# Performance work log

Hardware: AMD Instinct MI355X
Metric: run time of the kernel (lower is better)

## Reference

```python
import jax, jax.numpy as jnp
import numpy as np

EPS = 1e-5
DIM = 128
SCALE = DIM ** (-0.5)


def setup_inputs() -> dict:
    key = jax.random.key(0)
    k1, k2, k3 = jax.random.split(key, 3)
    B, N, D = 2, 128 * 128, DIM
    Q = N // 4
    x = jax.random.normal(k1, (B, N, D), dtype=jnp.float32)
    gamma = jnp.ones((D,), dtype=jnp.float32)
    beta = jnp.zeros((D,), dtype=jnp.float32)
    queries = jax.random.normal(k2, (Q, D), dtype=jnp.float32)
    W = jax.random.normal(k3, (2 * D, D), dtype=jnp.float32) * (1.0 / np.sqrt(D))
    return {"x": x, "gamma": gamma, "beta": beta, "queries": queries, "W": W}


def reference(x, gamma, beta, queries, W):
    # LayerNorm over last dim (eps matches torch default 1e-5)
    mu = jnp.mean(x, axis=-1, keepdims=True)
    var = jnp.mean(jnp.square(x - mu), axis=-1, keepdims=True)
    xn = (x - mu) * jax.lax.rsqrt(var + EPS) * gamma + beta  # [B, N, D]
    # learned-query cross attention: sim = Q @ xn^T * scale -> softmax -> @ xn
    sim = jnp.einsum('qd,bnd->bqn', queries, xn) * SCALE     # [B, Q, N]
    attn = jax.nn.softmax(sim, axis=-1)
    out = jnp.einsum('bqn,bnd->bqd', attn, xn)               # [B, Q, D]
    # trailing linear: dim -> 2*dim, no bias
    return jnp.einsum('bqd,ed->bqe', out, W)                 # [B, Q, 2D]
```

## Files before the change

kernel.cpp:

```cpp
#include <hip/hip_runtime.h>
#include <stdint.h>

#define Bb 2
#define Nn 16384
#define Dd 128
#define Qq 4096
#define Ee 256
#define NSPLIT 8
#define NCHUNK 2048
#define KV 64
#define NITER 32

typedef __bf16 bf16x8 __attribute__((ext_vector_type(8)));
typedef float floatx4 __attribute__((ext_vector_type(4)));

__device__ __forceinline__ unsigned f2bf1(float f) {
  unsigned u = __float_as_uint(f);
  u = u + 0x7FFFu + ((u >> 16) & 1u);
  return u >> 16;
}
__device__ __forceinline__ unsigned f2bf2(float lo, float hi) {
  return f2bf1(lo) | (f2bf1(hi) << 16);
}

__global__ __launch_bounds__(256) void k_ln(const float* __restrict__ x,
    const float* __restrict__ gamma, const float* __restrict__ beta,
    unsigned* __restrict__ xn) {
  int row = blockIdx.x * 4 + (threadIdx.x >> 6);
  int lane = threadIdx.x & 63;
  float2 v = ((const float2*)x)[(size_t)row * 64 + lane];
  float s = v.x + v.y, s2 = v.x * v.x + v.y * v.y;
#pragma unroll
  for (int off = 32; off; off >>= 1) {
    s += __shfl_xor(s, off);
    s2 += __shfl_xor(s2, off);
  }
  float mu = s * (1.0f / 128.0f);
  float var = s2 * (1.0f / 128.0f) - mu * mu;
  float rs = rsqrtf(var + 1e-5f);
  float2 g = ((const float2*)gamma)[lane];
  float2 bt = ((const float2*)beta)[lane];
  float y0 = (v.x - mu) * rs * g.x + bt.x;
  float y1 = (v.y - mu) * rs * g.y + bt.y;
  xn[(size_t)row * 64 + lane] = f2bf2(y0, y1);
}

__global__ __launch_bounds__(256) void k_cast(const float* __restrict__ queries,
    const float* __restrict__ W, unsigned short* __restrict__ qb,
    unsigned short* __restrict__ wb) {
  int i = blockIdx.x * 256 + threadIdx.x;
  const float QSC = 0.08838834764831845f * 1.4426950408889634f;
  if (i < Qq * Dd) {
    qb[i] = (unsigned short)f2bf1(queries[i] * QSC);
  } else {
    int j = i - Qq * Dd;
    if (j < Ee * Dd) wb[j] = (unsigned short)f2bf1(W[j]);
  }
}

#define TSTRIDE 132
__global__ __launch_bounds__(256) void k_transpose(
    const unsigned short* __restrict__ xn, unsigned short* __restrict__ xnT) {
  __shared__ unsigned short lds[64 * TSTRIDE];
  int bid = blockIdx.x;
  int b = bid >> 8, nt = bid & 255;
  int n0 = nt * 64;
  int t = threadIdx.x;
#pragma unroll
  for (int p = 0; p < 4; ++p) {
    int u = p * 256 + t;
    int r = u >> 4, c = u & 15;
    uint4 d4 = *(const uint4*)(xn + ((size_t)(b * Nn + n0 + r) * Dd + c * 8));
    uint2* dst = (uint2*)&lds[r * TSTRIDE + c * 8];
    dst[0] = make_uint2(d4.x, d4.y);
    dst[1] = make_uint2(d4.z, d4.w);
  }
  __syncthreads();
#pragma unroll
  for (int p = 0; p < 4; ++p) {
    int u = p * 256 + t;
    int dr = u >> 3, nc = u & 7;
    unsigned short e0 = lds[(nc * 8 + 0) * TSTRIDE + dr];
    unsigned short e1 = lds[(nc * 8 + 1) * TSTRIDE + dr];
    unsigned short e2 = lds[(nc * 8 + 2) * TSTRIDE + dr];
    unsigned short e3 = lds[(nc * 8 + 3) * TSTRIDE + dr];
    unsigned short e4 = lds[(nc * 8 + 4) * TSTRIDE + dr];
    unsigned short e5 = lds[(nc * 8 + 5) * TSTRIDE + dr];
    unsigned short e6 = lds[(nc * 8 + 6) * TSTRIDE + dr];
    unsigned short e7 = lds[(nc * 8 + 7) * TSTRIDE + dr];
    uint4 o;
    o.x = (unsigned)e0 | ((unsigned)e1 << 16);
    o.y = (unsigned)e2 | ((unsigned)e3 << 16);
    o.z = (unsigned)e4 | ((unsigned)e5 << 16);
    o.w = (unsigned)e6 | ((unsigned)e7 << 16);
    *(uint4*)(xnT + ((size_t)(b * Dd + dr) * Nn + n0 + nc * 8)) = o;
  }
}

__global__ __launch_bounds__(512, 2) void k_attn(
    const unsigned short* __restrict__ xn,
    const unsigned short* __restrict__ xnT,
    const unsigned short* __restrict__ qb,
    float* __restrict__ o_part,
    float* __restrict__ l_part) {
  __shared__ uint4 lds_x[1024];
  __shared__ uint4 lds_xt[1024];
  __shared__ uint4 lds_p[2048];

  const int bid = blockIdx.x;
  const int split = bid & 7, qt = (bid >> 3) & 15, b = bid >> 7;
  const int tid = threadIdx.x;
  const int wave = tid >> 6, lane = tid & 63;
  const int col = lane & 15, quad = lane >> 4;
  const int cs = col & 7;
  const int qwbase = qt * 256 + wave * 32;

  bf16x8 qf[2][4];
#pragma unroll
  for (int nt = 0; nt < 2; ++nt)
#pragma unroll
    for (int s = 0; s < 4; ++s)
      qf[nt][s] = *(const bf16x8*)(qb + (size_t)(qwbase + nt * 16 + col) * Dd + s * 32 + quad * 8);

  const floatx4 fz = {0.f, 0.f, 0.f, 0.f};
  floatx4 O[2][8];
#pragma unroll
  for (int a = 0; a < 2; ++a)
#pragma unroll
    for (int d = 0; d < 8; ++d) O[a][d] = fz;
  float lsum0 = 0.f, lsum1 = 0.f;

  const uint4* gx = (const uint4*)(xn + (size_t)b * Nn * Dd);
  const uint4* gxt = (const uint4*)(xnT + (size_t)b * Dd * Nn);

  for (int i = 0; i < NITER; ++i) {
    const int nb = split * NCHUNK + i * KV;
#pragma unroll
    for (int p = 0; p < 2; ++p) {
      int u = p * 512 + tid;
      int r = u >> 4, c = u & 15;
      lds_x[r * 16 + (c ^ (r & 7))] = gx[(size_t)(nb + r) * 16 + c];
    }
#pragma unroll
    for (int p = 0; p < 2; ++p) {
      int u = p * 512 + tid;
      int d = u >> 3, c = u & 7;
      lds_xt[d * 8 + (c ^ (d & 7))] = gxt[(size_t)d * (Nn / 8) + (nb / 8) + c];
    }
    __syncthreads();

    floatx4 S[4][2];
#pragma unroll
    for (int mt = 0; mt < 4; ++mt) {
      S[mt][0] = fz;
      S[mt][1] = fz;
    }
#pragma unroll
    for (int s = 0; s < 4; ++s) {
#pragma unroll
      for (int mt = 0; mt < 4; ++mt) {
        bf16x8 ax = *(const bf16x8*)&lds_x[(16 * mt + col) * 16 + ((4 * s + quad) ^ cs)];
        S[mt][0] = __builtin_amdgcn_mfma_f32_16x16x32_bf16(ax, qf[0][s], S[mt][0], 0, 0, 0);
        S[mt][1] = __builtin_amdgcn_mfma_f32_16x16x32_bf16(ax, qf[1][s], S[mt][1], 0, 0, 0);
      }
    }

#pragma unroll
    for (int nt = 0; nt < 2; ++nt) {
#pragma unroll
      for (int mt = 0; mt < 4; ++mt) {
        float p0 = exp2f(S[mt][nt][0]);
        float p1 = exp2f(S[mt][nt][1]);
        float p2 = exp2f(S[mt][nt][2]);
        float p3 = exp2f(S[mt][nt][3]);
        float ps = (p0 + p1) + (p2 + p3);
        if (nt == 0) lsum0 += ps; else lsum1 += ps;
        uint2 pk = make_uint2(f2bf2(p0, p1), f2bf2(p2, p3));
        *(uint2*)((char*)lds_p + wave * 4096 + (nt * 16 + col) * 128 +
                  (((2 * mt + (quad >> 1)) ^ cs) * 16) + 8 * (quad & 1)) = pk;
      }
    }

#pragma unroll
    for (int s2 = 0; s2 < 2; ++s2) {
      bf16x8 ap0 = *(const bf16x8*)((char*)lds_p + wave * 4096 + col * 128 +
                                    (((4 * s2 + quad) ^ cs) * 16));
      bf16x8 ap1 = *(const bf16x8*)((char*)lds_p + wave * 4096 + (16 + col) * 128 +
                                    (((4 * s2 + quad) ^ cs) * 16));
#pragma unroll
      for (int dn = 0; dn < 8; ++dn) {
        bf16x8 bx = *(const bf16x8*)&lds_xt[(16 * dn + col) * 8 + ((4 * s2 + quad) ^ cs)];
        O[0][dn] = __builtin_amdgcn_mfma_f32_16x16x32_bf16(ap0, bx, O[0][dn], 0, 0, 0);
        O[1][dn] = __builtin_amdgcn_mfma_f32_16x16x32_bf16(ap1, bx, O[1][dn], 0, 0, 0);
      }
    }
    __syncthreads();
  }

  float lt0 = lsum0 + __shfl_xor(lsum0, 16);
  lt0 += __shfl_xor(lt0, 32);
  float lt1 = lsum1 + __shfl_xor(lsum1, 16);
  lt1 += __shfl_xor(lt1, 32);
  if (quad == 0) {
    size_t lb = (size_t)(b * NSPLIT + split) * Qq + qwbase;
    l_part[lb + col] = lt0;
    l_part[lb + 16 + col] = lt1;
  }
#pragma unroll
  for (int mt2 = 0; mt2 < 2; ++mt2)
#pragma unroll
    for (int dn = 0; dn < 8; ++dn)
#pragma unroll
      for (int r = 0; r < 4; ++r) {
        int q = qwbase + mt2 * 16 + quad * 4 + r;
        o_part[((size_t)(b * NSPLIT + split) * Qq + q) * Dd + dn * 16 + col] = O[mt2][dn][r];
      }
}

__global__ __launch_bounds__(256) void k_comb(
    const float* __restrict__ o_part, const float* __restrict__ l_part,
    const unsigned short* __restrict__ wb, float* __restrict__ out) {
  __shared__ unsigned short lds_a[128 * 136];
  __shared__ float lds_linv[128];
  const int bid = blockIdx.x;
  const int b = bid >> 5, qc = bid & 31;
  const int qbase = qc * 128;
  const int tid = threadIdx.x;
  const int wave = tid >> 6, lane = tid & 63;
  const int col = lane & 15, quad = lane >> 4;

  if (tid < 128) {
    float l = 0.f;
#pragma unroll
    for (int s = 0; s < 8; ++s)
      l += l_part[(size_t)(b * 8 + s) * Qq + qbase + tid];
    lds_linv[tid] = 1.0f / l;
  }
  __syncthreads();

#pragma unroll
  for (int i = 0; i < 16; ++i) {
    int idx = i * 256 + tid;
    int q = idx >> 5, d4 = idx & 31;
    float4 acc = make_float4(0.f, 0.f, 0.f, 0.f);
#pragma unroll
    for (int s = 0; s < 8; ++s) {
      float4 v = *(const float4*)(o_part + ((size_t)(b * 8 + s) * Qq + qbase + q) * Dd + d4 * 4);
      acc.x += v.x; acc.y += v.y; acc.z += v.z; acc.w += v.w;
    }
    float li = lds_linv[q];
    uint2 pk = make_uint2(f2bf2(acc.x * li, acc.y * li), f2bf2(acc.z * li, acc.w * li));
    *(uint2*)((char*)lds_a + ((size_t)q * 136 + d4 * 4) * 2) = pk;
  }
  __syncthreads();

  bf16x8 af[2][4];
#pragma unroll
  for (int mt = 0; mt < 2; ++mt)
#pragma unroll
    for (int s = 0; s < 4; ++s)
      af[mt][s] = *(const bf16x8*)&lds_a[(wave * 32 + mt * 16 + col) * 136 + s * 32 + quad * 8];

  const floatx4 fz = {0.f, 0.f, 0.f, 0.f};
#pragma unroll
  for (int en = 0; en < 16; ++en) {
    floatx4 C0 = fz, C1 = fz;
#pragma unroll
    for (int s = 0; s < 4; ++s) {
      bf16x8 bw = *(const bf16x8*)(wb + (size_t)(en * 16 + col) * Dd + s * 32 + quad * 8);
      C0 = __builtin_amdgcn_mfma_f32_16x16x32_bf16(af[0][s], bw, C0, 0, 0, 0);
      C1 = __builtin_amdgcn_mfma_f32_16x16x32_bf16(af[1][s], bw, C1, 0, 0, 0);
    }
#pragma unroll
    for (int r = 0; r < 4; ++r) {
      int q0 = qbase + wave * 32 + quad * 4 + r;
      out[((size_t)b * Qq + q0) * Ee + en * 16 + col] = C0[r];
      out[((size_t)b * Qq + q0 + 16) * Ee + en * 16 + col] = C1[r];
    }
  }
}

extern "C" void kernel_launch(void* const* d_in, const int* in_sizes, int n_in,
                              void* d_out, int out_size, void* d_ws, size_t ws_size,
                              hipStream_t stream) {
  const float* x = (const float*)d_in[0];
  const float* gamma = (const float*)d_in[1];
  const float* beta = (const float*)d_in[2];
  const float* queries = (const float*)d_in[3];
  const float* W = (const float*)d_in[4];
  float* out = (float*)d_out;

  char* w = (char*)d_ws;
  unsigned short* xn = (unsigned short*)(w);
  unsigned short* xnT = (unsigned short*)(w + 8388608);
  unsigned short* qb = (unsigned short*)(w + 16777216);
  unsigned short* wb = (unsigned short*)(w + 17825792);
  float* o_part = (float*)(w + 17891328);
  float* l_part = (float*)(w + 51445760);

  k_ln<<<dim3(8192), dim3(256), 0, stream>>>(x, gamma, beta, (unsigned*)xn);
  k_cast<<<dim3(2176), dim3(256), 0, stream>>>(queries, W, qb, wb);
  k_transpose<<<dim3(512), dim3(256), 0, stream>>>(xn, xnT);
  k_attn<<<dim3(256), dim3(512), 0, stream>>>(xn, xnT, qb, o_part, l_part);
  k_comb<<<dim3(64), dim3(256), 0, stream>>>(o_part, l_part, wb, out);
}
```

Baseline: 194.7 us.

## Fuse layernorm, transpose and casts; halve attention query tile for more blocks

Merges the layernorm, bf16 cast of queries/W, and the xn transpose into one kernel that transposes from registers through LDS. This removes two launches and the extra global round trip of xn. The attention kernel now gives each wave 16 queries instead of 32 and launches twice as many blocks, with a higher occupancy hint, to fill more CUs. The trade-off is that each block reloads the K/V tiles for half as many queries, doubling global and LDS traffic per query. Float-to-bf16 conversion is changed to a cheaper round-half-up perm, and the exp uses the hardware exp2 builtin; both can shift numerics slightly.

```diff
diff --git a/kernel.cpp b/kernel.cpp
--- a/kernel.cpp
+++ b/kernel.cpp
@@ -1,7 +1,6 @@
 #include <hip/hip_runtime.h>
 #include <stdint.h>
 
-#define Bb 2
 #define Nn 16384
 #define Dd 128
 #define Qq 4096
@@ -14,90 +13,99 @@
 typedef __bf16 bf16x8 __attribute__((ext_vector_type(8)));
 typedef float floatx4 __attribute__((ext_vector_type(4)));
 
-__device__ __forceinline__ unsigned f2bf1(float f) {
-  unsigned u = __float_as_uint(f);
-  u = u + 0x7FFFu + ((u >> 16) & 1u);
-  return u >> 16;
-}
-__device__ __forceinline__ unsigned f2bf2(float lo, float hi) {
-  return f2bf1(lo) | (f2bf1(hi) << 16);
-}
-
-__global__ __launch_bounds__(256) void k_ln(const float* __restrict__ x,
-    const float* __restrict__ gamma, const float* __restrict__ beta,
-    unsigned* __restrict__ xn) {
-  int row = blockIdx.x * 4 + (threadIdx.x >> 6);
-  int lane = threadIdx.x & 63;
-  float2 v = ((const float2*)x)[(size_t)row * 64 + lane];
-  float s = v.x + v.y, s2 = v.x * v.x + v.y * v.y;
-#pragma unroll
-  for (int off = 32; off; off >>= 1) {
-    s += __shfl_xor(s, off);
-    s2 += __shfl_xor(s2, off);
-  }
+__device__ __forceinline__ float fexp2(float x) {
+#if __has_builtin(__builtin_amdgcn_exp2f)
+  return __builtin_amdgcn_exp2f(x);
+#else
+  return exp2f(x);
+#endif
+}
+__device__ __forceinline__ unsigned pk_bf(float lo, float hi) {
+  return __builtin_amdgcn_perm(__float_as_uint(hi) + 0x8000u,
+                               __float_as_uint(lo) + 0x8000u, 0x07060302u);
+}
+__device__ __forceinline__ unsigned short bf1(float f) {
+  return (unsigned short)((__float_as_uint(f) + 0x8000u) >> 16);
+}
+
+__global__ __launch_bounds__(256) void k_lnt(
+    const float* __restrict__ x, const float* __restrict__ gamma,
+    const float* __restrict__ beta, const float* __restrict__ queries,
+    const float* __restrict__ W, unsigned* __restrict__ xn,
+    unsigned short* __restrict__ xnT, unsigned short* __restrict__ qb,
+    unsigned short* __restrict__ wb) {
+  __shared__ uint2 lds2[64 * 32];
+  const int tid = threadIdx.x;
+  const int bid = blockIdx.x;
+  const int b = bid >> 8, n0 = (bid & 255) * 64;
+  const int r = tid >> 2, qd = tid & 3;
+
+  const float4* xp = (const float4*)(x + ((size_t)(b * Nn + n0 + r)) * Dd + qd * 32);
+  float4 v[8];
+  float s = 0.f, s2 = 0.f;
+#pragma unroll
+  for (int i = 0; i < 8; ++i) {
+    v[i] = xp[i];
+    s += (v[i].x + v[i].y) + (v[i].z + v[i].w);
+    s2 += (v[i].x * v[i].x + v[i].y * v[i].y) + (v[i].z * v[i].z + v[i].w * v[i].w);
+  }
+  s += __shfl_xor(s, 1); s2 += __shfl_xor(s2, 1);
+  s += __shfl_xor(s, 2); s2 += __shfl_xor(s2, 2);
   float mu = s * (1.0f / 128.0f);
   float var = s2 * (1.0f / 128.0f) - mu * mu;
   float rs = rsqrtf(var + 1e-5f);
-  float2 g = ((const float2*)gamma)[lane];
-  float2 bt = ((const float2*)beta)[lane];
-  float y0 = (v.x - mu) * rs * g.x + bt.x;
-  float y1 = (v.y - mu) * rs * g.y + bt.y;
-  xn[(size_t)row * 64 + lane] = f2bf2(y0, y1);
-}
-
-__global__ __launch_bounds__(256) void k_cast(const float* __restrict__ queries,
-    const float* __restrict__ W, unsigned short* __restrict__ qb,
-    unsigned short* __restrict__ wb) {
-  int i = blockIdx.x * 256 + threadIdx.x;
+
+  const float4* gp = (const float4*)(gamma + qd * 32);
+  const float4* bp = (const float4*)(beta + qd * 32);
+  unsigned pk[16];
+#pragma unroll
+  for (int i = 0; i < 8; ++i) {
+    float4 g = gp[i], bt = bp[i];
+    float y0 = (v[i].x - mu) * rs * g.x + bt.x;
+    float y1 = (v[i].y - mu) * rs * g.y + bt.y;
+    float y2 = (v[i].z - mu) * rs * g.z + bt.z;
+    float y3 = (v[i].w - mu) * rs * g.w + bt.w;
+    pk[2 * i] = pk_bf(y0, y1);
+    pk[2 * i + 1] = pk_bf(y2, y3);
+  }
+  uint4* xo = (uint4*)(xn + ((size_t)(b * Nn + n0 + r)) * 64 + qd * 16);
+#pragma unroll
+  for (int i = 0; i < 4; ++i)
+    xo[i] = make_uint4(pk[4 * i], pk[4 * i + 1], pk[4 * i + 2], pk[4 * i + 3]);
+  const int rk = r & 31;
+#pragma unroll
+  for (int kk = 0; kk < 8; ++kk)
+    lds2[r * 32 + ((qd * 8 + kk) ^ rk)] = make_uint2(pk[2 * kk], pk[2 * kk + 1]);
+  __syncthreads();
+  const int dq = tid >> 3, nc = tid & 7;
+  uint2 U[8];
+#pragma unroll
+  for (int j = 0; j < 8; ++j) {
+    int rr = nc * 8 + j;
+    U[j] = lds2[rr * 32 + (dq ^ (rr & 31))];
+  }
+#pragma unroll
+  for (int e = 0; e < 4; ++e) {
+    unsigned a0 = (e & 2) ? U[0].y : U[0].x, a1 = (e & 2) ? U[1].y : U[1].x;
+    unsigned a2 = (e & 2) ? U[2].y : U[2].x, a3 = (e & 2) ? U[3].y : U[3].x;
+    unsigned a4 = (e & 2) ? U[4].y : U[4].x, a5 = (e & 2) ? U[5].y : U[5].x;
+    unsigned a6 = (e & 2) ? U[6].y : U[6].x, a7 = (e & 2) ? U[7].y : U[7].x;
+    unsigned sel = (e & 1) ? 0x07060302u : 0x05040100u;
+    uint4 o;
+    o.x = __builtin_amdgcn_perm(a1, a0, sel);
+    o.y = __builtin_amdgcn_perm(a3, a2, sel);
+    o.z = __builtin_amdgcn_perm(a5, a4, sel);
+    o.w = __builtin_amdgcn_perm(a7, a6, sel);
+    *(uint4*)(xnT + ((size_t)(b * Dd + dq * 4 + e)) * Nn + n0 + nc * 8) = o;
+  }
   const float QSC = 0.08838834764831845f * 1.4426950408889634f;
-  if (i < Qq * Dd) {
-    qb[i] = (unsigned short)f2bf1(queries[i] * QSC);
-  } else {
-    int j = i - Qq * Dd;
-    if (j < Ee * Dd) wb[j] = (unsigned short)f2bf1(W[j]);
-  }
-}
-
-#define TSTRIDE 132
-__global__ __launch_bounds__(256) void k_transpose(
-    const unsigned short* __restrict__ xn, unsigned short* __restrict__ xnT) {
-  __shared__ unsigned short lds[64 * TSTRIDE];
-  int bid = blockIdx.x;
-  int b = bid >> 8, nt = bid & 255;
-  int n0 = nt * 64;
-  int t = threadIdx.x;
-#pragma unroll
-  for (int p = 0; p < 4; ++p) {
-    int u = p * 256 + t;
-    int r = u >> 4, c = u & 15;
-    uint4 d4 = *(const uint4*)(xn + ((size_t)(b * Nn + n0 + r) * Dd + c * 8));
-    uint2* dst = (uint2*)&lds[r * TSTRIDE + c * 8];
-    dst[0] = make_uint2(d4.x, d4.y);
-    dst[1] = make_uint2(d4.z, d4.w);
-  }
-  __syncthreads();
-#pragma unroll
-  for (int p = 0; p < 4; ++p) {
-    int u = p * 256 + t;
-    int dr = u >> 3, nc = u & 7;
-    unsigned short e0 = lds[(nc * 8 + 0) * TSTRIDE + dr];
-    unsigned short e1 = lds[(nc * 8 + 1) * TSTRIDE + dr];
-    unsigned short e2 = lds[(nc * 8 + 2) * TSTRIDE + dr];
-    unsigned short e3 = lds[(nc * 8 + 3) * TSTRIDE + dr];
-    unsigned short e4 = lds[(nc * 8 + 4) * TSTRIDE + dr];
-    unsigned short e5 = lds[(nc * 8 + 5) * TSTRIDE + dr];
-    unsigned short e6 = lds[(nc * 8 + 6) * TSTRIDE + dr];
-    unsigned short e7 = lds[(nc * 8 + 7) * TSTRIDE + dr];
-    uint4 o;
-    o.x = (unsigned)e0 | ((unsigned)e1 << 16);
-    o.y = (unsigned)e2 | ((unsigned)e3 << 16);
-    o.z = (unsigned)e4 | ((unsigned)e5 << 16);
-    o.w = (unsigned)e6 | ((unsigned)e7 << 16);
-    *(uint4*)(xnT + ((size_t)(b * Dd + dr) * Nn + n0 + nc * 8)) = o;
-  }
-}
-
-__global__ __launch_bounds__(512, 2) void k_attn(
+  for (int idx = bid * 256 + tid; idx < Qq * Dd + Ee * Dd; idx += 512 * 256) {
+    if (idx < Qq * Dd) qb[idx] = bf1(queries[idx] * QSC);
+    else wb[idx - Qq * Dd] = bf1(W[idx - Qq * Dd]);
+  }
+}
+
+__global__ __launch_bounds__(512, 4) void k_attn(
     const unsigned short* __restrict__ xn,
     const unsigned short* __restrict__ xnT,
     const unsigned short* __restrict__ qb,
@@ -105,30 +113,26 @@
     float* __restrict__ l_part) {
   __shared__ uint4 lds_x[1024];
   __shared__ uint4 lds_xt[1024];
-  __shared__ uint4 lds_p[2048];
+  __shared__ char lds_p[16384];
 
   const int bid = blockIdx.x;
-  const int split = bid & 7, qt = (bid >> 3) & 15, b = bid >> 7;
+  const int split = bid & 7, qt = (bid >> 3) & 31, b = bid >> 8;
   const int tid = threadIdx.x;
   const int wave = tid >> 6, lane = tid & 63;
   const int col = lane & 15, quad = lane >> 4;
   const int cs = col & 7;
-  const int qwbase = qt * 256 + wave * 32;
-
-  bf16x8 qf[2][4];
-#pragma unroll
-  for (int nt = 0; nt < 2; ++nt)
-#pragma unroll
-    for (int s = 0; s < 4; ++s)
-      qf[nt][s] = *(const bf16x8*)(qb + (size_t)(qwbase + nt * 16 + col) * Dd + s * 32 + quad * 8);
+  const int qwbase = qt * 128 + wave * 16;
+
+  bf16x8 qf[4];
+#pragma unroll
+  for (int s = 0; s < 4; ++s)
+    qf[s] = *(const bf16x8*)(qb + (size_t)(qwbase + col) * Dd + s * 32 + quad * 8);
 
   const floatx4 fz = {0.f, 0.f, 0.f, 0.f};
-  floatx4 O[2][8];
-#pragma unroll
-  for (int a = 0; a < 2; ++a)
-#pragma unroll
-    for (int d = 0; d < 8; ++d) O[a][d] = fz;
-  float lsum0 = 0.f, lsum1 = 0.f;
+  floatx4 O[8];
+#pragma unroll
+  for (int d = 0; d < 8; ++d) O[d] = fz;
+  float lsum = 0.f;
 
   const uint4* gx = (const uint4*)(xn + (size_t)b * Nn * Dd);
   const uint4* gxt = (const uint4*)(xnT + (size_t)b * Dd * Nn);
@@ -138,8 +142,8 @@
 #pragma unroll
     for (int p = 0; p < 2; ++p) {
       int u = p * 512 + tid;
-      int r = u >> 4, c = u & 15;
-      lds_x[r * 16 + (c ^ (r & 7))] = gx[(size_t)(nb + r) * 16 + c];
+      int rr = u >> 4, c = u & 15;
+      lds_x[rr * 16 + (c ^ (rr & 7))] = gx[(size_t)(nb + rr) * 16 + c];
     }
 #pragma unroll
     for (int p = 0; p < 2; ++p) {
@@ -149,87 +153,68 @@
     }
     __syncthreads();
 
-    floatx4 S[4][2];
-#pragma unroll
-    for (int mt = 0; mt < 4; ++mt) {
-      S[mt][0] = fz;
-      S[mt][1] = fz;
-    }
-#pragma unroll
-    for (int s = 0; s < 4; ++s) {
+    floatx4 S[4];
+#pragma unroll
+    for (int mt = 0; mt < 4; ++mt) S[mt] = fz;
+#pragma unroll
+    for (int s = 0; s < 4; ++s)
 #pragma unroll
       for (int mt = 0; mt < 4; ++mt) {
         bf16x8 ax = *(const bf16x8*)&lds_x[(16 * mt + col) * 16 + ((4 * s + quad) ^ cs)];
-        S[mt][0] = __builtin_amdgcn_mfma_f32_16x16x32_bf16(ax, qf[0][s], S[mt][0], 0, 0, 0);
-        S[mt][1] = __builtin_amdgcn_mfma_f32_16x16x32_bf16(ax, qf[1][s], S[mt][1], 0, 0, 0);
+        S[mt] = __builtin_amdgcn_mfma_f32_16x16x32_bf16(ax, qf[s], S[mt], 0, 0, 0);
       }
-    }
-
-#pragma unroll
-    for (int nt = 0; nt < 2; ++nt) {
-#pragma unroll
-      for (int mt = 0; mt < 4; ++mt) {
-        float p0 = exp2f(S[mt][nt][0]);
-        float p1 = exp2f(S[mt][nt][1]);
-        float p2 = exp2f(S[mt][nt][2]);
-        float p3 = exp2f(S[mt][nt][3]);
-        float ps = (p0 + p1) + (p2 + p3);
-        if (nt == 0) lsum0 += ps; else lsum1 += ps;
-        uint2 pk = make_uint2(f2bf2(p0, p1), f2bf2(p2, p3));
-        *(uint2*)((char*)lds_p + wave * 4096 + (nt * 16 + col) * 128 +
-                  (((2 * mt + (quad >> 1)) ^ cs) * 16) + 8 * (quad & 1)) = pk;
-      }
+
+#pragma unroll
+    for (int mt = 0; mt < 4; ++mt) {
+      float p0 = fexp2(S[mt][0]);
+      float p1 = fexp2(S[mt][1]);
+      float p2 = fexp2(S[mt][2]);
+      float p3 = fexp2(S[mt][3]);
+      lsum += (p0 + p1) + (p2 + p3);
+      *(uint2*)(lds_p + wave * 2048 + col * 128 +
+                (((2 * mt + (quad >> 1)) ^ cs) * 16) + (quad & 1) * 8) =
+          make_uint2(pk_bf(p0, p1), pk_bf(p2, p3));
     }
 
 #pragma unroll
     for (int s2 = 0; s2 < 2; ++s2) {
-      bf16x8 ap0 = *(const bf16x8*)((char*)lds_p + wave * 4096 + col * 128 +
-                                    (((4 * s2 + quad) ^ cs) * 16));
-      bf16x8 ap1 = *(const bf16x8*)((char*)lds_p + wave * 4096 + (16 + col) * 128 +
-                                    (((4 * s2 + quad) ^ cs) * 16));
+      bf16x8 ap = *(const bf16x8*)(lds_p + wave * 2048 + col * 128 +
+                                   (((4 * s2 + quad) ^ cs) * 16));
 #pragma unroll
       for (int dn = 0; dn < 8; ++dn) {
         bf16x8 bx = *(const bf16x8*)&lds_xt[(16 * dn + col) * 8 + ((4 * s2 + quad) ^ cs)];
-        O[0][dn] = __builtin_amdgcn_mfma_f32_16x16x32_bf16(ap0, bx, O[0][dn], 0, 0, 0);
-        O[1][dn] = __builtin_amdgcn_mfma_f32_16x16x32_bf16(ap1, bx, O[1][dn], 0, 0, 0);
+        O[dn] = __builtin_amdgcn_mfma_f32_16x16x32_bf16(ap, bx, O[dn], 0, 0, 0);
       }
     }
     __syncthreads();
   }
 
-  float lt0 = lsum0 + __shfl_xor(lsum0, 16);
-  lt0 += __shfl_xor(lt0, 32);
-  float lt1 = lsum1 + __shfl_xor(lsum1, 16);
-  lt1 += __shfl_xor(lt1, 32);
-  if (quad == 0) {
-    size_t lb = (size_t)(b * NSPLIT + split) * Qq + qwbase;
-    l_part[lb + col] = lt0;
-    l_part[lb + 16 + col] = lt1;
-  }
-#pragma unroll
-  for (int mt2 = 0; mt2 < 2; ++mt2)
-#pragma unroll
-    for (int dn = 0; dn < 8; ++dn)
-#pragma unroll
-      for (int r = 0; r < 4; ++r) {
-        int q = qwbase + mt2 * 16 + quad * 4 + r;
-        o_part[((size_t)(b * NSPLIT + split) * Qq + q) * Dd + dn * 16 + col] = O[mt2][dn][r];
-      }
+  float lt = lsum + __shfl_xor(lsum, 16);
+  lt += __shfl_xor(lt, 32);
+  if (quad == 0)
+    l_part[(size_t)(b * NSPLIT + split) * Qq + qwbase + col] = lt;
+#pragma unroll
+  for (int dn = 0; dn < 8; ++dn)
+#pragma unroll
+    for (int r = 0; r < 4; ++r) {
+      int q = qwbase + quad * 4 + r;
+      o_part[((size_t)(b * NSPLIT + split) * Qq + q) * Dd + dn * 16 + col] = O[dn][r];
+    }
 }
 
 __global__ __launch_bounds__(256) void k_comb(
     const float* __restrict__ o_part, const float* __restrict__ l_part,
     const unsigned short* __restrict__ wb, float* __restrict__ out) {
-  __shared__ unsigned short lds_a[128 * 136];
-  __shared__ float lds_linv[128];
+  __shared__ unsigned short lds_a[64 * 136];
+  __shared__ float lds_linv[64];
   const int bid = blockIdx.x;
-  const int b = bid >> 5, qc = bid & 31;
-  const int qbase = qc * 128;
+  const int b = bid >> 6, qc = bid & 63;
+  const int qbase = qc * 64;
   const int tid = threadIdx.x;
   const int wave = tid >> 6, lane = tid & 63;
   const int col = lane & 15, quad = lane >> 4;
 
-  if (tid < 128) {
+  if (tid < 64) {
     float l = 0.f;
 #pragma unroll
     for (int s = 0; s < 8; ++s)
@@ -239,7 +224,7 @@
   __syncthreads();
 
 #pragma unroll
-  for (int i = 0; i < 16; ++i) {
+  for (int i = 0; i < 8; ++i) {
     int idx = i * 256 + tid;
     int q = idx >> 5, d4 = idx & 31;
     float4 acc = make_float4(0.f, 0.f, 0.f, 0.f);
@@ -249,33 +234,29 @@
       acc.x += v.x; acc.y += v.y; acc.z += v.z; acc.w += v.w;
     }
     float li = lds_linv[q];
-    uint2 pk = make_uint2(f2bf2(acc.x * li, acc.y * li), f2bf2(acc.z * li, acc.w * li));
-    *(uint2*)((char*)lds_a + ((size_t)q * 136 + d4 * 4) * 2) = pk;
+    *(uint2*)((char*)lds_a + (size_t)q * 272 + d4 * 8) =
+        make_uint2(pk_bf(acc.x * li, acc.y * li), pk_bf(acc.z * li, acc.w * li));
   }
   __syncthreads();
 
-  bf16x8 af[2][4];
-#pragma unroll
-  for (int mt = 0; mt < 2; ++mt)
-#pragma unroll
-    for (int s = 0; s < 4; ++s)
-      af[mt][s] = *(const bf16x8*)&lds_a[(wave * 32 + mt * 16 + col) * 136 + s * 32 + quad * 8];
+  bf16x8 af[4];
+#pragma unroll
+  for (int s = 0; s < 4; ++s)
+    af[s] = *(const bf16x8*)&lds_a[(wave * 16 + col) * 136 + s * 32 + quad * 8];
 
   const floatx4 fz = {0.f, 0.f, 0.f, 0.f};
 #pragma unroll
   for (int en = 0; en < 16; ++en) {
-    floatx4 C0 = fz, C1 = fz;
+    floatx4 C = fz;
 #pragma unroll
     for (int s = 0; s < 4; ++s) {
       bf16x8 bw = *(const bf16x8*)(wb + (size_t)(en * 16 + col) * Dd + s * 32 + quad * 8);
-      C0 = __builtin_amdgcn_mfma_f32_16x16x32_bf16(af[0][s], bw, C0, 0, 0, 0);
-      C1 = __builtin_amdgcn_mfma_f32_16x16x32_bf16(af[1][s], bw, C1, 0, 0, 0);
+      C = __builtin_amdgcn_mfma_f32_16x16x32_bf16(af[s], bw, C, 0, 0, 0);
     }
 #pragma unroll
     for (int r = 0; r < 4; ++r) {
-      int q0 = qbase + wave * 32 + quad * 4 + r;
-      out[((size_t)b * Qq + q0) * Ee + en * 16 + col] = C0[r];
-      out[((size_t)b * Qq + q0 + 16) * Ee + en * 16 + col] = C1[r];
+      int q0 = qbase + wave * 16 + quad * 4 + r;
+      out[((size_t)b * Qq + q0) * Ee + en * 16 + col] = C[r];
     }
   }
 }
@@ -298,9 +279,8 @@
   float* o_part = (float*)(w + 17891328);
   float* l_part = (float*)(w + 51445760);
 
-  k_ln<<<dim3(8192), dim3(256), 0, stream>>>(x, gamma, beta, (unsigned*)xn);
-  k_cast<<<dim3(2176), dim3(256), 0, stream>>>(queries, W, qb, wb);
-  k_transpose<<<dim3(512), dim3(256), 0, stream>>>(xn, xnT);
-  k_attn<<<dim3(256), dim3(512), 0, stream>>>(xn, xnT, qb, o_part, l_part);
-  k_comb<<<dim3(64), dim3(256), 0, stream>>>(o_part, l_part, wb, out);
-}
+  k_lnt<<<dim3(512), dim3(256), 0, stream>>>(x, gamma, beta, queries, W,
+                                             (unsigned*)xn, xnT, qb, wb);
+  k_attn<<<dim3(512), dim3(512), 0, stream>>>(xn, xnT, qb, o_part, l_part);
+  k_comb<<<dim3(128), dim3(256), 0, stream>>>(o_part, l_part, wb, out);
+}
```

Result: faster. 185.6 us (-4.7%).
